# Kernel optimization log

Hardware: AMD Instinct MI355X
Metric: run time of the kernel (lower is better)

Reference implementation:

```python
import jax, jax.numpy as jnp
import numpy as np

NUM_EMBEDDINGS = 1024
EMBEDDING_DIM = 256
COMMITMENT_COST = 0.25


def setup_inputs() -> dict:
    key = jax.random.key(0)
    k_z, k_e = jax.random.split(key)
    z = jax.random.normal(k_z, (8, EMBEDDING_DIM, 16, 16, 16), dtype=jnp.float32)
    # nn.Embedding weight initialized uniform(-1/K, 1/K)
    codebook = jax.random.uniform(
        k_e, (NUM_EMBEDDINGS, EMBEDDING_DIM), dtype=jnp.float32,
        minval=-1.0 / NUM_EMBEDDINGS, maxval=1.0 / NUM_EMBEDDINGS)
    return {"z": z, "codebook": codebook}


def reference(z, codebook):
    B, D, H, W, L = z.shape
    # (B, D, H, W, L) -> (B, H, W, L, D) -> (N, D)
    z_perm = jnp.transpose(z, (0, 2, 3, 4, 1))          # (B,H,W,L,D)
    z_flat = z_perm.reshape(-1, D)                       # (N,D)
    # squared-distance via expansion: ||z||^2 + ||e||^2 - 2 z.e^T
    distances = ((z_flat ** 2).sum(axis=1, keepdims=True)
                 + (codebook ** 2).sum(axis=1)
                 - 2.0 * z_flat @ codebook.T)            # (N,K)
    indices = jnp.argmin(distances, axis=1)              # (N,)
    quantized = codebook[indices].reshape(B, H, W, L, D)
    idx_out = indices.reshape(B, H, W, L)
    # losses (stop_gradient mirrors .detach())
    e_latent_loss = jnp.mean((jax.lax.stop_gradient(quantized) - z_perm) ** 2)
    q_latent_loss = jnp.mean((quantized - jax.lax.stop_gradient(z_perm)) ** 2)
    vq_loss = q_latent_loss + COMMITMENT_COST * e_latent_loss
    # straight-through estimator
    quant_st = z_perm + jax.lax.stop_gradient(quantized - z_perm)
    quant_out = jnp.transpose(quant_st, (0, 4, 1, 2, 3))  # (B,D,H,W,L)
    return quant_out, idx_out, vq_loss
```

## Files before the change

kernel.cpp:

```cpp
#include <hip/hip_runtime.h>


#define K_CODES 1024
#define DIM 256
#define N_TOK 32768
#define SPATIAL 4096
#define TOK_BLK 64
#define NBLK (N_TOK / TOK_BLK)
#define CAP 28
#define MARGIN 1e-3f

typedef __attribute__((ext_vector_type(8))) short short8;
typedef __attribute__((ext_vector_type(4))) float float4v;

#define WS_LOSS 0
#define WS_CNT 8
#define WS_E2 16
#define WS_EB 2048
#define WS_SZ 133120
#define WS_CAND 165888
#define WS_CCNT 624640

#define O_IDX (8 * DIM * SPATIAL)
#define O_LOSS (O_IDX + N_TOK)

__device__ __forceinline__ short f2bf(float v) {
  unsigned u = __float_as_uint(v);
  u = (u + 0x7fffu + ((u >> 16) & 1u)) >> 16;
  return (short)u;
}

__global__ __launch_bounds__(256) void prep_kernel(const float* __restrict__ e,
                                                   float* __restrict__ ws) {
  __shared__ float sq[DIM];
  __shared__ __align__(16) short sbf[DIM];
  __shared__ float chv[16];
  int k = blockIdx.x, d = threadIdx.x;
  float v = e[k * DIM + d];
  sbf[d] = f2bf(v);
  sq[d] = __fmul_rn(v, v);
  __syncthreads();
  if (d < 32) {
    int f = d >> 2, q = d & 3;
    int stage = k >> 6, ct = (k >> 4) & 3, nn = k & 15;
    short8 chunk = *(const short8*)(sbf + f * 32 + q * 8);
    int off8 = ((stage * 4 + ct) * 8 + f) * 64 + q * 16 + nn;
    ((short8*)(ws + WS_EB))[off8] = chunk;
  }
  if (d < 16) {
    int blkb = d >> 3, j = d & 7;
    const float* x = sq + blkb * 128;
    float c = x[j];
#pragma unroll
    for (int i = 1; i < 16; i++) c = __fadd_rn(c, x[i * 8 + j]);
    chv[d] = c;
  }
  __syncthreads();
  if (d == 0) {
    float a0 = __fadd_rn(__fadd_rn(chv[0], chv[1]), __fadd_rn(chv[2], chv[3]));
    float a1 = __fadd_rn(__fadd_rn(chv[4], chv[5]), __fadd_rn(chv[6], chv[7]));
    float resA = __fadd_rn(a0, a1);
    float b0 = __fadd_rn(__fadd_rn(chv[8], chv[9]), __fadd_rn(chv[10], chv[11]));
    float b1 = __fadd_rn(__fadd_rn(chv[12], chv[13]), __fadd_rn(chv[14], chv[15]));
    float resB = __fadd_rn(b0, b1);
    ws[WS_E2 + k] = __fadd_rn(resA, resB);
    if (k == 0) {
      ws[WS_LOSS] = 0.f;
      ((unsigned*)ws)[WS_CNT] = 0u;
    }
  }
}

__global__ __launch_bounds__(512, 4) void filter_kernel(const float* __restrict__ z,
                                                        float* __restrict__ ws) {
  __shared__ __align__(16) short Bst[64 * 256];
  __shared__ unsigned short cand[TOK_BLK][CAP];
  __shared__ int cnt[TOK_BLK];
  __shared__ float Szp[2][TOK_BLK];

  int tid = threadIdx.x, w = tid >> 6, lane = tid & 63;
  int quad = lane >> 4, nn = lane & 15;
  int g = w & 3, kh = w >> 2;
  int n0 = blockIdx.x * TOK_BLK;
  int b = n0 >> 12, s0 = n0 & 4095;
  const float* zb = z + (size_t)b * DIM * SPATIAL + s0;
  const float* Se = ws + WS_E2;
  const uint4* eBg = (const uint4*)(ws + WS_EB);
  if (tid < TOK_BLK) cnt[tid] = 0;

  {
    const float* zp = zb + g * 16 + nn;
    float r0, r1;
    {
      int j0 = quad * 2;
      float v0 = zp[(size_t)(kh * 128 + j0) * SPATIAL];
      float v1 = zp[(size_t)(kh * 128 + j0 + 1) * SPATIAL];
      r0 = __fmul_rn(v0, v0);
      r1 = __fmul_rn(v1, v1);
      for (int i = 1; i < 16; i++) {
        v0 = zp[(size_t)(kh * 128 + i * 8 + j0) * SPATIAL];
        v1 = zp[(size_t)(kh * 128 + i * 8 + j0 + 1) * SPATIAL];
        r0 = __fadd_rn(r0, __fmul_rn(v0, v0));
        r1 = __fadd_rn(r1, __fmul_rn(v1, v1));
      }
    }
    float p = __fadd_rn(r0, r1);
    float s1 = __fadd_rn(p, __shfl_xor(p, 16));
    float s2 = __fadd_rn(s1, __shfl_xor(s1, 32));
    if (quad == 0) Szp[kh][g * 16 + nn] = s2;
  }

  int tokA = g * 16 + nn;
  short8 A[8];
#pragma unroll
  for (int f = 0; f < 8; f++) {
    short8 a;
#pragma unroll
    for (int j = 0; j < 8; j++) {
      int d = f * 32 + quad * 8 + j;
      a[j] = f2bf(zb[(size_t)d * SPATIAL + tokA]);
    }
    A[f] = a;
  }

  float thr[4] = {3.4e38f, 3.4e38f, 3.4e38f, 3.4e38f};
  for (int stage = 0; stage < 16; stage++) {
    __syncthreads();
#pragma unroll
    for (int i = 0; i < 4; i++)
      ((uint4*)Bst)[i * 512 + tid] = eBg[(size_t)stage * 2048 + i * 512 + tid];
    __syncthreads();

    int ct0 = kh * 2, ct1 = kh * 2 + 1;
    int kbase0 = stage * 64 + ct0 * 16;
    int kbase1 = stage * 64 + ct1 * 16;
    float4v C0 = {0.f, 0.f, 0.f, 0.f};
    float4v C1 = {0.f, 0.f, 0.f, 0.f};
    const short8* Bp0 = (const short8*)Bst + ct0 * 8 * 64;
    const short8* Bp1 = (const short8*)Bst + ct1 * 8 * 64;
#pragma unroll
    for (int f = 0; f < 8; f++) {
      short8 B0 = Bp0[f * 64 + lane];
      short8 B1 = Bp1[f * 64 + lane];
      C0 = __builtin_amdgcn_mfma_f32_16x16x32_bf16(A[f], B0, C0, 0, 0, 0);
      C1 = __builtin_amdgcn_mfma_f32_16x16x32_bf16(A[f], B1, C1, 0, 0, 0);
    }
    float SeK0 = Se[kbase0 + nn];
    float SeK1 = Se[kbase1 + nn];
    float s0v[4], s1v[4], m0[4], m1[4];
#pragma unroll
    for (int r = 0; r < 4; r++) {
      s0v[r] = fmaf(-2.f, C0[r], SeK0);
      s1v[r] = fmaf(-2.f, C1[r], SeK1);
      m0[r] = s0v[r];
      m1[r] = s1v[r];
    }
#pragma unroll
    for (int dlt = 1; dlt <= 8; dlt <<= 1) {
#pragma unroll
      for (int r = 0; r < 4; r++) {
        m0[r] = fminf(m0[r], __shfl_xor(m0[r], dlt, 16));
        m1[r] = fminf(m1[r], __shfl_xor(m1[r], dlt, 16));
      }
    }
    bool pr[4];
#pragma unroll
    for (int r = 0; r < 4; r++) {
      thr[r] = fminf(thr[r], m0[r]);
      pr[r] = s0v[r] < thr[r] + MARGIN;
    }
    if (__ballot(pr[0] | pr[1] | pr[2] | pr[3])) {
#pragma unroll
      for (int r = 0; r < 4; r++) {
        unsigned long long bl = __ballot(pr[r]);
        unsigned grp = (unsigned)((bl >> (quad * 16)) & 0xffffULL);
        if (grp) {
          int tb = g * 16 + quad * 4 + r;
          int base = 0;
          if (nn == 0) base = atomicAdd(&cnt[tb], __popc(grp));
          base = __shfl(base, quad * 16);
          if (pr[r]) {
            int pos = base + __popc(grp & ((1u << nn) - 1u));
            if (pos < CAP) cand[tb][pos] = (unsigned short)(kbase0 + nn);
          }
        }
      }
    }
#pragma unroll
    for (int r = 0; r < 4; r++) {
      thr[r] = fminf(thr[r], m1[r]);
      pr[r] = s1v[r] < thr[r] + MARGIN;
    }
    if (__ballot(pr[0] | pr[1] | pr[2] | pr[3])) {
#pragma unroll
      for (int r = 0; r < 4; r++) {
        unsigned long long bl = __ballot(pr[r]);
        unsigned grp = (unsigned)((bl >> (quad * 16)) & 0xffffULL);
        if (grp) {
          int tb = g * 16 + quad * 4 + r;
          int base = 0;
          if (nn == 0) base = atomicAdd(&cnt[tb], __popc(grp));
          base = __shfl(base, quad * 16);
          if (pr[r]) {
            int pos = base + __popc(grp & ((1u << nn) - 1u));
            if (pos < CAP) cand[tb][pos] = (unsigned short)(kbase1 + nn);
          }
        }
      }
    }
  }
  __syncthreads();

  {
    int t = tid >> 3, j = tid & 7;
    int cv = cnt[t];
    if (j == 0) ((int*)ws)[WS_CCNT + n0 + t] = cv;
    if (j == 1)
      ws[WS_SZ + n0 + t] = __fadd_rn(Szp[0][t], Szp[1][t]);
    int cl = cv < CAP ? cv : CAP;
    unsigned short* cg = (unsigned short*)(ws + WS_CAND) + (size_t)(n0 + t) * CAP;
    for (int c = j; c < cl; c += 8) cg[c] = cand[t][c];
  }
}

__global__ __launch_bounds__(256, 8) void recheck_kernel(const float* __restrict__ z,
                                                         const float* __restrict__ e,
                                                         float* __restrict__ ws,
                                                         float* __restrict__ out) {
  int tid = threadIdx.x, w = tid >> 6, lane = tid & 63;
  int tl = lane >> 3, oct = lane & 7;
  int n0 = blockIdx.x * 32;
  int b = n0 >> 12, s0 = n0 & 4095;
  const float* zb = z + (size_t)b * DIM * SPATIAL + s0;
  const float* Se = ws + WS_E2;
  const unsigned short* candg = (const unsigned short*)(ws + WS_CAND);
  const int* cntg = (const int*)ws + WS_CCNT;

  int tb = w * 8 + tl;
  int tok = n0 + tb;
  int cc = cntg[tok];
  int cl = cc < CAP ? cc : CAP;
  float Szn = ws[WS_SZ + tok];
  float bestD = 3.4e38f;
  int bestk = 0x7fffffff;
  {
    const float* zp = zb + tb;
    const unsigned short* cg = candg + (size_t)tok * CAP;
    for (int c = oct; c < cl; c += 8) {
      int k = cg[c];
      const float* er = e + (size_t)k * DIM;
      float acc = 0.f;
#pragma unroll 4
      for (int dd = 0; dd < DIM; dd += 4) {
        float4 e4 = *(const float4*)(er + dd);
        acc = fmaf(zp[(size_t)(dd + 0) * SPATIAL], e4.x, acc);
        acc = fmaf(zp[(size_t)(dd + 1) * SPATIAL], e4.y, acc);
        acc = fmaf(zp[(size_t)(dd + 2) * SPATIAL], e4.z, acc);
        acc = fmaf(zp[(size_t)(dd + 3) * SPATIAL], e4.w, acc);
      }
      float D = __fsub_rn(__fadd_rn(Szn, Se[k]), __fmul_rn(2.f, acc));
      if (D < bestD || (D == bestD && k < bestk)) { bestD = D; bestk = k; }
    }
  }
#pragma unroll
  for (int off = 4; off >= 1; off >>= 1) {
    float oD = __shfl_down(bestD, off, 8);
    int ok = __shfl_down(bestk, off, 8);
    if (oD < bestD || (oD == bestD && ok < bestk)) { bestD = oD; bestk = ok; }
  }
  if (oct == 0 && cc <= CAP) out[O_IDX + tok] = (float)bestk;
  for (int t = 0; t < 8; t++) {
    int tb2 = w * 8 + t;
    if (cntg[n0 + tb2] > CAP) {
      const float* zq = zb + tb2;
      float Sz2 = ws[WS_SZ + n0 + tb2];
      float bD = 3.4e38f;
      int bk = 0x7fffffff;
      for (int k = lane; k < K_CODES; k += 64) {
        const float* er = e + (size_t)k * DIM;
        float acc = 0.f;
#pragma unroll 4
        for (int dd = 0; dd < DIM; dd += 4) {
          float4 e4 = *(const float4*)(er + dd);
          acc = fmaf(zq[(size_t)(dd + 0) * SPATIAL], e4.x, acc);
          acc = fmaf(zq[(size_t)(dd + 1) * SPATIAL], e4.y, acc);
          acc = fmaf(zq[(size_t)(dd + 2) * SPATIAL], e4.z, acc);
          acc = fmaf(zq[(size_t)(dd + 3) * SPATIAL], e4.w, acc);
        }
        float D = __fsub_rn(__fadd_rn(Sz2, Se[k]), __fmul_rn(2.f, acc));
        if (D < bD || (D == bD && k < bk)) { bD = D; bk = k; }
      }
#pragma unroll
      for (int m = 1; m < 64; m <<= 1) {
        float oD = __shfl_xor(bD, m);
        int ok = __shfl_xor(bk, m);
        if (oD < bD || (oD == bD && ok < bk)) { bD = oD; bk = ok; }
      }
      if (lane == 0) out[O_IDX + n0 + tb2] = (float)bk;
    }
  }
}

__global__ __launch_bounds__(256, 4) void epilogue_kernel(const float* __restrict__ z,
                                                          const float* __restrict__ e,
                                                          float* __restrict__ ws,
                                                          float* __restrict__ out) {
  __shared__ float red[4];
  int tid = threadIdx.x, w = tid >> 6, lane = tid & 63;
  int n0 = blockIdx.x * TOK_BLK;
  int b = n0 >> 12, s0 = n0 & 4095;
  const float* zb = z + (size_t)b * DIM * SPATIAL + s0;
  int mten = (int)out[O_IDX + n0 + lane];
  const float* erow = e + (size_t)mten * DIM;
  float* op = out + (size_t)b * DIM * SPATIAL + s0;
  float sumsq = 0.f;
#pragma unroll 4
  for (int i4 = 0; i4 < 64; i4 += 4) {
    int d = w * 64 + i4;
    float4 v4 = *(const float4*)(erow + d);
#pragma unroll
    for (int m = 0; m < 4; m++) {
      float v = (m == 0) ? v4.x : (m == 1) ? v4.y : (m == 2) ? v4.z : v4.w;
      float zv = zb[(size_t)(d + m) * SPATIAL + lane];
      float df = __fsub_rn(v, zv);
      sumsq = fmaf(df, df, sumsq);
      op[(size_t)(d + m) * SPATIAL + lane] = v;
    }
  }
#pragma unroll
  for (int o = 32; o > 0; o >>= 1) sumsq += __shfl_down(sumsq, o, 64);
  if (lane == 0) red[w] = sumsq;
  __syncthreads();
  if (tid == 0) {
    atomicAdd(ws + WS_LOSS, red[0] + red[1] + red[2] + red[3]);
    __threadfence();
    unsigned t = atomicAdd((unsigned*)ws + WS_CNT, 1u);
    if (t == NBLK - 1) {
      float total = atomicAdd(ws + WS_LOSS, 0.f);
      out[O_LOSS] = 1.25f * total / 8388608.f;
    }
  }
}

extern "C" void kernel_launch(void* const* d_in, const int* in_sizes, int n_in,
                              void* d_out, int out_size, void* d_ws, size_t ws_size,
                              hipStream_t stream) {
  const float* z = (const float*)d_in[0];
  const float* e = (const float*)d_in[1];
  float* ws = (float*)d_ws;
  float* out = (float*)d_out;

  prep_kernel<<<K_CODES, 256, 0, stream>>>(e, ws);
  filter_kernel<<<NBLK, 512, 0, stream>>>(z, ws);
  recheck_kernel<<<N_TOK / 32, 256, 0, stream>>>(z, e, ws, out);
  epilogue_kernel<<<NBLK, 256, 0, stream>>>(z, e, ws, out);
}
```

Before: 234.9 us.

## Fuse recheck and epilogue kernels with transposed z tile staged in LDS

```diff
diff --git a/kernel.cpp b/kernel.cpp
--- a/kernel.cpp
+++ b/kernel.cpp
@@ -9,6 +9,7 @@
 #define NBLK (N_TOK / TOK_BLK)
 #define CAP 28
 #define MARGIN 1e-3f
+#define ZLD 257
 
 typedef __attribute__((ext_vector_type(8))) short short8;
 typedef __attribute__((ext_vector_type(4))) float float4v;
@@ -223,19 +224,35 @@
   }
 }
 
-__global__ __launch_bounds__(256, 8) void recheck_kernel(const float* __restrict__ z,
-                                                         const float* __restrict__ e,
-                                                         float* __restrict__ ws,
-                                                         float* __restrict__ out) {
+__global__ __launch_bounds__(512, 4) void de_kernel(const float* __restrict__ z,
+                                                    const float* __restrict__ e,
+                                                    float* __restrict__ ws,
+                                                    float* __restrict__ out) {
+  __shared__ float zs[TOK_BLK * ZLD];
+  __shared__ int mini_sh[TOK_BLK];
+  __shared__ float red[8];
+
   int tid = threadIdx.x, w = tid >> 6, lane = tid & 63;
-  int tl = lane >> 3, oct = lane & 7;
-  int n0 = blockIdx.x * 32;
+  int n0 = blockIdx.x * TOK_BLK;
   int b = n0 >> 12, s0 = n0 & 4095;
   const float* zb = z + (size_t)b * DIM * SPATIAL + s0;
   const float* Se = ws + WS_E2;
   const unsigned short* candg = (const unsigned short*)(ws + WS_CAND);
   const int* cntg = (const int*)ws + WS_CCNT;
 
+#pragma unroll
+  for (int it = 0; it < 8; it++) {
+    int c = it * 512 + tid;
+    int d = c >> 4, t4 = (c & 15) << 2;
+    float4 v4 = *(const float4*)(zb + (size_t)d * SPATIAL + t4);
+    zs[(t4 + 0) * ZLD + d] = v4.x;
+    zs[(t4 + 1) * ZLD + d] = v4.y;
+    zs[(t4 + 2) * ZLD + d] = v4.z;
+    zs[(t4 + 3) * ZLD + d] = v4.w;
+  }
+  __syncthreads();
+
+  int tl = lane >> 3, oct = lane & 7;
   int tb = w * 8 + tl;
   int tok = n0 + tb;
   int cc = cntg[tok];
@@ -244,7 +261,7 @@
   float bestD = 3.4e38f;
   int bestk = 0x7fffffff;
   {
-    const float* zp = zb + tb;
+    const float* zp = zs + tb * ZLD;
     const unsigned short* cg = candg + (size_t)tok * CAP;
     for (int c = oct; c < cl; c += 8) {
       int k = cg[c];
@@ -253,10 +270,10 @@
 #pragma unroll 4
       for (int dd = 0; dd < DIM; dd += 4) {
         float4 e4 = *(const float4*)(er + dd);
-        acc = fmaf(zp[(size_t)(dd + 0) * SPATIAL], e4.x, acc);
-        acc = fmaf(zp[(size_t)(dd + 1) * SPATIAL], e4.y, acc);
-        acc = fmaf(zp[(size_t)(dd + 2) * SPATIAL], e4.z, acc);
-        acc = fmaf(zp[(size_t)(dd + 3) * SPATIAL], e4.w, acc);
+        acc = fmaf(zp[dd + 0], e4.x, acc);
+        acc = fmaf(zp[dd + 1], e4.y, acc);
+        acc = fmaf(zp[dd + 2], e4.z, acc);
+        acc = fmaf(zp[dd + 3], e4.w, acc);
       }
       float D = __fsub_rn(__fadd_rn(Szn, Se[k]), __fmul_rn(2.f, acc));
       if (D < bestD || (D == bestD && k < bestk)) { bestD = D; bestk = k; }
@@ -268,11 +285,14 @@
     int ok = __shfl_down(bestk, off, 8);
     if (oD < bestD || (oD == bestD && ok < bestk)) { bestD = oD; bestk = ok; }
   }
-  if (oct == 0 && cc <= CAP) out[O_IDX + tok] = (float)bestk;
+  if (oct == 0 && cc <= CAP) {
+    mini_sh[tb] = bestk;
+    out[O_IDX + tok] = (float)bestk;
+  }
   for (int t = 0; t < 8; t++) {
     int tb2 = w * 8 + t;
     if (cntg[n0 + tb2] > CAP) {
-      const float* zq = zb + tb2;
+      const float* zq = zs + tb2 * ZLD;
       float Sz2 = ws[WS_SZ + n0 + tb2];
       float bD = 3.4e38f;
       int bk = 0x7fffffff;
@@ -282,10 +302,10 @@
 #pragma unroll 4
         for (int dd = 0; dd < DIM; dd += 4) {
           float4 e4 = *(const float4*)(er + dd);
-          acc = fmaf(zq[(size_t)(dd + 0) * SPATIAL], e4.x, acc);
-          acc = fmaf(zq[(size_t)(dd + 1) * SPATIAL], e4.y, acc);
-          acc = fmaf(zq[(size_t)(dd + 2) * SPATIAL], e4.z, acc);
-          acc = fmaf(zq[(size_t)(dd + 3) * SPATIAL], e4.w, acc);
+          acc = fmaf(zq[dd + 0], e4.x, acc);
+          acc = fmaf(zq[dd + 1], e4.y, acc);
+          acc = fmaf(zq[dd + 2], e4.z, acc);
+          acc = fmaf(zq[dd + 3], e4.w, acc);
         }
         float D = __fsub_rn(__fadd_rn(Sz2, Se[k]), __fmul_rn(2.f, acc));
         if (D < bD || (D == bD && k < bk)) { bD = D; bk = k; }
@@ -296,32 +316,27 @@
         int ok = __shfl_xor(bk, m);
         if (oD < bD || (oD == bD && ok < bk)) { bD = oD; bk = ok; }
       }
-      if (lane == 0) out[O_IDX + n0 + tb2] = (float)bk;
-    }
-  }
-}
-
-__global__ __launch_bounds__(256, 4) void epilogue_kernel(const float* __restrict__ z,
-                                                          const float* __restrict__ e,
-                                                          float* __restrict__ ws,
-                                                          float* __restrict__ out) {
-  __shared__ float red[4];
-  int tid = threadIdx.x, w = tid >> 6, lane = tid & 63;
-  int n0 = blockIdx.x * TOK_BLK;
-  int b = n0 >> 12, s0 = n0 & 4095;
-  const float* zb = z + (size_t)b * DIM * SPATIAL + s0;
-  int mten = (int)out[O_IDX + n0 + lane];
+      if (lane == 0) {
+        mini_sh[tb2] = bk;
+        out[O_IDX + n0 + tb2] = (float)bk;
+      }
+    }
+  }
+  __syncthreads();
+
+  int mten = mini_sh[lane];
   const float* erow = e + (size_t)mten * DIM;
+  const float* zrow = zs + lane * ZLD;
   float* op = out + (size_t)b * DIM * SPATIAL + s0;
   float sumsq = 0.f;
-#pragma unroll 4
-  for (int i4 = 0; i4 < 64; i4 += 4) {
-    int d = w * 64 + i4;
+#pragma unroll 2
+  for (int i4 = 0; i4 < 32; i4 += 4) {
+    int d = w * 32 + i4;
     float4 v4 = *(const float4*)(erow + d);
 #pragma unroll
     for (int m = 0; m < 4; m++) {
       float v = (m == 0) ? v4.x : (m == 1) ? v4.y : (m == 2) ? v4.z : v4.w;
-      float zv = zb[(size_t)(d + m) * SPATIAL + lane];
+      float zv = zrow[d + m];
       float df = __fsub_rn(v, zv);
       sumsq = fmaf(df, df, sumsq);
       op[(size_t)(d + m) * SPATIAL + lane] = v;
@@ -332,7 +347,9 @@
   if (lane == 0) red[w] = sumsq;
   __syncthreads();
   if (tid == 0) {
-    atomicAdd(ws + WS_LOSS, red[0] + red[1] + red[2] + red[3]);
+    float rs = ((red[0] + red[1]) + (red[2] + red[3])) +
+               ((red[4] + red[5]) + (red[6] + red[7]));
+    atomicAdd(ws + WS_LOSS, rs);
     __threadfence();
     unsigned t = atomicAdd((unsigned*)ws + WS_CNT, 1u);
     if (t == NBLK - 1) {
@@ -352,6 +369,5 @@
 
   prep_kernel<<<K_CODES, 256, 0, stream>>>(e, ws);
   filter_kernel<<<NBLK, 512, 0, stream>>>(z, ws);
-  recheck_kernel<<<N_TOK / 32, 256, 0, stream>>>(z, e, ws, out);
-  epilogue_kernel<<<NBLK, 256, 0, stream>>>(z, e, ws, out);
-}
+  de_kernel<<<NBLK, 512, 0, stream>>>(z, e, ws, out);
+}
```

New measurement: 205.2 us. 1.14x faster.
